# Optimization experiments

Measured on AMD Instinct MI355X. Metric: run time of the kernel, lower is better.

## Reference

```python
import jax, jax.numpy as jnp
import numpy as np

F_DIM = 128
H_DIM = 64
N_NODES = 100000
N_EDGES = 1000000
BN_EPS = 1e-5

def setup_inputs() -> dict:
    key = jax.random.key(0)
    ks = jax.random.split(key, 10)
    x = jax.random.normal(ks[0], (N_NODES, F_DIM), dtype=jnp.float32)
    edges = jax.random.randint(ks[1], (2, N_EDGES), 0, N_NODES, dtype=jnp.int64)
    s_in = 1.0 / np.sqrt(2 * F_DIM)
    s_h = 1.0 / np.sqrt(H_DIM)
    W_in = jax.random.uniform(ks[2], (H_DIM, 2 * F_DIM), jnp.float32, -s_in, s_in)
    b_in = jax.random.uniform(ks[3], (H_DIM,), jnp.float32, -s_in, s_in)
    W_h = jax.random.uniform(ks[4], (H_DIM, H_DIM), jnp.float32, -s_h, s_h)
    b_h = jax.random.uniform(ks[5], (H_DIM,), jnp.float32, -s_h, s_h)
    gamma = jnp.ones((H_DIM,), jnp.float32)
    beta = jnp.zeros((H_DIM,), jnp.float32)
    W_out = jax.random.uniform(ks[6], (1, H_DIM), jnp.float32, -s_h, s_h)
    b_out = jax.random.uniform(ks[7], (1,), jnp.float32, -s_h, s_h)
    return {"x": x, "edges": edges, "W_in": W_in, "b_in": b_in,
            "W_h": W_h, "b_h": b_h, "gamma": gamma, "beta": beta,
            "W_out": W_out, "b_out": b_out}

def reference(x, edges, W_in, b_in, W_h, b_h, gamma, beta, W_out, b_out):
    # gather node pair features and concat -> [E, 2F]
    ef = jnp.concatenate((x[edges[0]], x[edges[1]]), axis=1)
    h = jax.nn.relu(ef @ W_in.T + b_in)          # [E, H]
    h = h @ W_h.T + b_h                           # hidden linear
    # BatchNorm1d in training mode: batch stats over edge dim (biased var)
    mean = jnp.mean(h, axis=0)
    var = jnp.mean((h - mean) ** 2, axis=0)
    h = (h - mean) * jax.lax.rsqrt(var + BN_EPS) * gamma + beta
    h = jax.nn.relu(h)
    edge_scores = (h @ W_out.T + b_out).squeeze(-1)  # [E]
    return edge_scores
```

## Files before the change

### kernel.cpp

```cpp
#include <hip/hip_runtime.h>
#include <hip/hip_bf16.h>
#include <hip/hip_fp16.h>

#define N_NODES 100000
#define N_EDGES 1000000
#define BN_EPS 1e-5f
#define N_CHUNKS (N_EDGES / 64)

typedef __attribute__((ext_vector_type(8))) short bf16x8;
typedef __attribute__((ext_vector_type(4))) float f32x4;


__device__ __forceinline__ unsigned pk2(float a, float b) {
  unsigned ua = __builtin_bit_cast(unsigned, a);
  unsigned ub = __builtin_bit_cast(unsigned, b);
  ua += 0x7fffu + ((ua >> 16) & 1u);
  ub += 0x7fffu + ((ub >> 16) & 1u);
  return (ua >> 16) | (ub & 0xffff0000u);
}

__device__ __forceinline__ bf16x8 pack8(float4 v0, float4 v1) {
  uint4 u = make_uint4(pk2(v0.x, v0.y), pk2(v0.z, v0.w), pk2(v1.x, v1.y), pk2(v1.z, v1.w));
  return __builtin_bit_cast(bf16x8, u);
}

__device__ __forceinline__ bf16x8 frag_relu_add(uint4 a, uint4 d) {
  uint4 r;
  const unsigned* aw = (const unsigned*)&a;
  const unsigned* dw = (const unsigned*)&d;
  unsigned* rw = (unsigned*)&r;
#pragma unroll
  for (int q = 0; q < 4; ++q) {
    const float alo = __builtin_bit_cast(float, aw[q] << 16);
    const float ahi = __builtin_bit_cast(float, aw[q] & 0xffff0000u);
    const float dlo = __builtin_bit_cast(float, dw[q] << 16);
    const float dhi = __builtin_bit_cast(float, dw[q] & 0xffff0000u);
    rw[q] = pk2(fmaxf(alo + dlo, 0.f), fmaxf(ahi + dhi, 0.f));
  }
  return __builtin_bit_cast(bf16x8, r);
}

__device__ __forceinline__ void load_bfr(const float* __restrict__ W_h, int l15, int l4,
                                         bf16x8 bfr[4][2]) {
#pragma unroll
  for (int nt = 0; nt < 4; ++nt)
#pragma unroll
    for (int kk = 0; kk < 2; ++kk) {
      const float* wp = W_h + (16 * nt + l15) * 64 + (kk * 4 + l4) * 8;
      bfr[nt][kk] = pack8(*(const float4*)wp, *(const float4*)(wp + 4));
    }
}

__global__ __launch_bounds__(64) void k_probe(const unsigned* __restrict__ eu,
                                              int* __restrict__ flag) {
  if (threadIdx.x == 0) {
    unsigned acc = 0;
#pragma unroll
    for (int i = 1; i < 64; i += 2) acc |= eu[i];
    *flag = (acc == 0) ? 1 : 0;
  }
}

__global__ __launch_bounds__(256) void k1_mfma(
    const float* __restrict__ x, const float* __restrict__ W_in,
    const float* __restrict__ b_in, __hip_bfloat16* __restrict__ A,
    float* __restrict__ stats) {
  const int t = threadIdx.x;
  if (blockIdx.x == 0 && t < 128) stats[t] = 0.f;
  const int lane = t & 63;
  const int w = t >> 6;
  const int l15 = lane & 15, l4 = lane >> 4;
  const int nb = blockIdx.x * 128 + (w >> 1) * 64;
  const int cb = (w & 1) * 64;

  bf16x8 wfrag[4][4];
#pragma unroll
  for (int ct = 0; ct < 4; ++ct) {
#pragma unroll
    for (int kk = 0; kk < 4; ++kk) {
      const float* wp = W_in + (16 * ct + l15) * 256 + (cb ? 128 : 0) + 32 * kk + 8 * l4;
      wfrag[ct][kk] = pack8(*(const float4*)wp, *(const float4*)(wp + 4));
    }
  }
  f32x4 acc[4][4];
#pragma unroll
  for (int nt = 0; nt < 4; ++nt)
#pragma unroll
    for (int ct = 0; ct < 4; ++ct)
      acc[nt][ct] = (f32x4){0.f, 0.f, 0.f, 0.f};

#pragma unroll
  for (int nt = 0; nt < 4; ++nt) {
    int node = nb + 16 * nt + l15;
    node = node < N_NODES ? node : N_NODES - 1;
    const float* xr = x + (size_t)node * 128 + 8 * l4;
#pragma unroll
    for (int kk = 0; kk < 4; ++kk) {
      const bf16x8 xf = pack8(*(const float4*)(xr + 32 * kk), *(const float4*)(xr + 32 * kk + 4));
#pragma unroll
      for (int ct = 0; ct < 4; ++ct)
        acc[nt][ct] = __builtin_amdgcn_mfma_f32_16x16x32_bf16(wfrag[ct][kk], xf, acc[nt][ct], 0, 0, 0);
    }
  }

  float4 bv[4];
#pragma unroll
  for (int ct = 0; ct < 4; ++ct)
    bv[ct] = cb ? make_float4(0.f, 0.f, 0.f, 0.f) : *(const float4*)(b_in + 16 * ct + 4 * l4);
#pragma unroll
  for (int nt = 0; nt < 4; ++nt) {
    const int node = nb + 16 * nt + l15;
    if (node < N_NODES) {
      __hip_bfloat16* ap = A + (size_t)node * 128 + cb + 4 * l4;
#pragma unroll
      for (int ct = 0; ct < 4; ++ct) {
        uint2 u;
        u.x = pk2(acc[nt][ct][0] + bv[ct].x, acc[nt][ct][1] + bv[ct].y);
        u.y = pk2(acc[nt][ct][2] + bv[ct].z, acc[nt][ct][3] + bv[ct].w);
        *(uint2*)(ap + 16 * ct) = u;
      }
    }
  }
}

template<bool STORE_G>
__global__ __launch_bounds__(256, 2) void k2_stats(
    const __hip_bfloat16* __restrict__ A, const void* __restrict__ edges,
    const int* __restrict__ flag, const float* __restrict__ W_h,
    float* __restrict__ stats, __half* __restrict__ g) {
  const int lane = threadIdx.x & 63;
  const int l15 = lane & 15, l4 = lane >> 4;
  bf16x8 bfr[4][2];
  load_bfr(W_h, l15, l4, bfr);

  const int is64 = *flag;
  const long long* e64 = (const long long*)edges;
  const int* e32 = (const int*)edges;
  float vs[4] = {0.f, 0.f, 0.f, 0.f};
  float vq[4] = {0.f, 0.f, 0.f, 0.f};
  const int gwave = blockIdx.x * 4 + (threadIdx.x >> 6);
  const int nwaves = gridDim.x * 4;

  for (int c = gwave; c < N_CHUNKS; c += 2 * nwaves) {
    const int cy = c + nwaves;
    const bool has2 = cy < N_CHUNKS;
    int sX[4], dX[4], sY[4], dY[4];
#pragma unroll
    for (int mt = 0; mt < 4; ++mt) {
      const int ex = c * 64 + mt * 16 + l15;
      if (is64) { sX[mt] = (int)e64[ex]; dX[mt] = (int)e64[N_EDGES + ex]; }
      else      { sX[mt] = e32[ex];      dX[mt] = e32[N_EDGES + ex]; }
    }
    const int cyc = has2 ? cy : c;
#pragma unroll
    for (int mt = 0; mt < 4; ++mt) {
      const int ey = cyc * 64 + mt * 16 + l15;
      if (is64) { sY[mt] = (int)e64[ey]; dY[mt] = (int)e64[N_EDGES + ey]; }
      else      { sY[mt] = e32[ey];      dY[mt] = e32[N_EDGES + ey]; }
    }
    uint4 xs0[4], xs1[4], xd0[4], xd1[4];
    uint4 ys0[4], ys1[4], yd0[4], yd1[4];
#pragma unroll
    for (int mt = 0; mt < 4; ++mt) {
      const uint4* As = (const uint4*)(A + (size_t)sX[mt] * 128);
      const uint4* Ad = (const uint4*)(A + (size_t)dX[mt] * 128 + 64);
      xs0[mt] = As[l4]; xs1[mt] = As[4 + l4];
      xd0[mt] = Ad[l4]; xd1[mt] = Ad[4 + l4];
    }
#pragma unroll
    for (int mt = 0; mt < 4; ++mt) {
      const uint4* As = (const uint4*)(A + (size_t)sY[mt] * 128);
      const uint4* Ad = (const uint4*)(A + (size_t)dY[mt] * 128 + 64);
      ys0[mt] = As[l4]; ys1[mt] = As[4 + l4];
      yd0[mt] = Ad[l4]; yd1[mt] = Ad[4 + l4];
    }
#pragma unroll
    for (int mt = 0; mt < 4; ++mt) {
      const bf16x8 a0 = frag_relu_add(xs0[mt], xd0[mt]);
      const bf16x8 a1 = frag_relu_add(xs1[mt], xd1[mt]);
#pragma unroll
      for (int nt = 0; nt < 4; ++nt) {
        f32x4 cc = {0.f, 0.f, 0.f, 0.f};
        cc = __builtin_amdgcn_mfma_f32_16x16x32_bf16(a0, bfr[nt][0], cc, 0, 0, 0);
        cc = __builtin_amdgcn_mfma_f32_16x16x32_bf16(a1, bfr[nt][1], cc, 0, 0, 0);
        if (STORE_G) {
          uint2 u;
          u.x = __builtin_bit_cast(unsigned, __floats2half2_rn(cc[0], cc[1]));
          u.y = __builtin_bit_cast(unsigned, __floats2half2_rn(cc[2], cc[3]));
          *(uint2*)(g + ((((size_t)c * 4 + mt) * 4 + nt) * 64 + lane) * 4) = u;
        }
#pragma unroll
        for (int j = 0; j < 4; ++j) { vs[nt] += cc[j]; vq[nt] += cc[j] * cc[j]; }
      }
    }
    if (has2) {
#pragma unroll
      for (int mt = 0; mt < 4; ++mt) {
        const bf16x8 a0 = frag_relu_add(ys0[mt], yd0[mt]);
        const bf16x8 a1 = frag_relu_add(ys1[mt], yd1[mt]);
#pragma unroll
        for (int nt = 0; nt < 4; ++nt) {
          f32x4 cc = {0.f, 0.f, 0.f, 0.f};
          cc = __builtin_amdgcn_mfma_f32_16x16x32_bf16(a0, bfr[nt][0], cc, 0, 0, 0);
          cc = __builtin_amdgcn_mfma_f32_16x16x32_bf16(a1, bfr[nt][1], cc, 0, 0, 0);
          if (STORE_G) {
            uint2 u;
            u.x = __builtin_bit_cast(unsigned, __floats2half2_rn(cc[0], cc[1]));
            u.y = __builtin_bit_cast(unsigned, __floats2half2_rn(cc[2], cc[3]));
            *(uint2*)(g + ((((size_t)cy * 4 + mt) * 4 + nt) * 64 + lane) * 4) = u;
          }
#pragma unroll
          for (int j = 0; j < 4; ++j) { vs[nt] += cc[j]; vq[nt] += cc[j] * cc[j]; }
        }
      }
    }
  }
#pragma unroll
  for (int nt = 0; nt < 4; ++nt) {
    float s1 = vs[nt], s2 = vq[nt];
    s1 += __shfl_xor(s1, 16, 64); s1 += __shfl_xor(s1, 32, 64);
    s2 += __shfl_xor(s2, 16, 64); s2 += __shfl_xor(s2, 32, 64);
    if (lane < 16) {
      atomicAdd(&stats[lane + 16 * nt], s1);
      atomicAdd(&stats[64 + lane + 16 * nt], s2);
    }
  }
}

__global__ __launch_bounds__(64) void k3_finalize(
    const float* __restrict__ stats, const float* __restrict__ gamma,
    const float* __restrict__ beta, float* __restrict__ ss) {
  const int c = threadIdx.x;
  if (c < 64) {
    const float inv_e = 1.f / (float)N_EDGES;
    const float mg = stats[c] * inv_e;
    const float var = stats[64 + c] * inv_e - mg * mg;
    const float scale = gamma[c] * rsqrtf(var + BN_EPS);
    ss[c] = scale;
    ss[64 + c] = beta[c] - scale * mg;
  }
}

__global__ __launch_bounds__(256) void k4_stream(
    const __half* __restrict__ g, const float* __restrict__ ss,
    const float* __restrict__ W_out, const float* __restrict__ b_out,
    float* __restrict__ out) {
  const int lane = threadIdx.x & 63;
  const int l15 = lane & 15, l4 = lane >> 4;
  float scl[4], shf[4], wo[4];
#pragma unroll
  for (int nt = 0; nt < 4; ++nt) {
    scl[nt] = ss[l15 + 16 * nt];
    shf[nt] = ss[64 + l15 + 16 * nt];
    wo[nt] = W_out[l15 + 16 * nt];
  }
  const float bo = b_out[0];
  const int gwave = blockIdx.x * 4 + (threadIdx.x >> 6);
  const int nwaves = gridDim.x * 4;
  for (int chunk = gwave; chunk < N_CHUNKS; chunk += nwaves) {
#pragma unroll
    for (int mt = 0; mt < 4; ++mt) {
      float t0 = 0.f, t1 = 0.f, t2 = 0.f, t3 = 0.f;
#pragma unroll
      for (int nt = 0; nt < 4; ++nt) {
        const uint2 u = *(const uint2*)(g + ((((size_t)chunk * 4 + mt) * 4 + nt) * 64 + lane) * 4);
        const __half2 h0 = __builtin_bit_cast(__half2, u.x);
        const __half2 h1 = __builtin_bit_cast(__half2, u.y);
        t0 += fmaxf(fmaf(__low2float(h0),  scl[nt], shf[nt]), 0.f) * wo[nt];
        t1 += fmaxf(fmaf(__high2float(h0), scl[nt], shf[nt]), 0.f) * wo[nt];
        t2 += fmaxf(fmaf(__low2float(h1),  scl[nt], shf[nt]), 0.f) * wo[nt];
        t3 += fmaxf(fmaf(__high2float(h1), scl[nt], shf[nt]), 0.f) * wo[nt];
      }
      const int ebase = chunk * 64 + mt * 16 + 4 * l4;
#pragma unroll
      for (int j = 0; j < 4; ++j) {
        float r = (j == 0) ? t0 : (j == 1) ? t1 : (j == 2) ? t2 : t3;
        r += __shfl_xor(r, 1, 64);
        r += __shfl_xor(r, 2, 64);
        r += __shfl_xor(r, 4, 64);
        r += __shfl_xor(r, 8, 64);
        if (l15 == 0) out[ebase + j] = r + bo;
      }
    }
  }
}

__global__ __launch_bounds__(256) void k4_gather(
    const __hip_bfloat16* __restrict__ A, const void* __restrict__ edges,
    const int* __restrict__ flag, const float* __restrict__ W_h,
    const float* __restrict__ ss, const float* __restrict__ W_out,
    const float* __restrict__ b_out, float* __restrict__ out) {
  const int lane = threadIdx.x & 63;
  const int l15 = lane & 15, l4 = lane >> 4;
  bf16x8 bfr[4][2];
  load_bfr(W_h, l15, l4, bfr);
  float scl[4], shf[4], wo[4];
#pragma unroll
  for (int nt = 0; nt < 4; ++nt) {
    scl[nt] = ss[l15 + 16 * nt];
    shf[nt] = ss[64 + l15 + 16 * nt];
    wo[nt] = W_out[l15 + 16 * nt];
  }
  const float bo = b_out[0];
  const int is64 = *flag;
  const long long* e64 = (const long long*)edges;
  const int* e32 = (const int*)edges;
  const int gwave = blockIdx.x * 4 + (threadIdx.x >> 6);
  const int nwaves = gridDim.x * 4;
  for (int chunk = gwave; chunk < N_CHUNKS; chunk += nwaves) {
    const int base = chunk * 64;
#pragma unroll
    for (int mt = 0; mt < 4; ++mt) {
      const int eidx = base + mt * 16 + l15;
      int s, d;
      if (is64) { s = (int)e64[eidx]; d = (int)e64[N_EDGES + eidx]; }
      else      { s = e32[eidx];      d = e32[N_EDGES + eidx]; }
      const uint4* As = (const uint4*)(A + (size_t)s * 128);
      const uint4* Ad = (const uint4*)(A + (size_t)d * 128 + 64);
      const bf16x8 a0 = frag_relu_add(As[l4], Ad[l4]);
      const bf16x8 a1 = frag_relu_add(As[4 + l4], Ad[4 + l4]);
      float t0 = 0.f, t1 = 0.f, t2 = 0.f, t3 = 0.f;
#pragma unroll
      for (int nt = 0; nt < 4; ++nt) {
        f32x4 cc = {0.f, 0.f, 0.f, 0.f};
        cc = __builtin_amdgcn_mfma_f32_16x16x32_bf16(a0, bfr[nt][0], cc, 0, 0, 0);
        cc = __builtin_amdgcn_mfma_f32_16x16x32_bf16(a1, bfr[nt][1], cc, 0, 0, 0);
        t0 += fmaxf(fmaf(cc[0], scl[nt], shf[nt]), 0.f) * wo[nt];
        t1 += fmaxf(fmaf(cc[1], scl[nt], shf[nt]), 0.f) * wo[nt];
        t2 += fmaxf(fmaf(cc[2], scl[nt], shf[nt]), 0.f) * wo[nt];
        t3 += fmaxf(fmaf(cc[3], scl[nt], shf[nt]), 0.f) * wo[nt];
      }
      const int ebase = base + mt * 16 + 4 * l4;
#pragma unroll
      for (int j = 0; j < 4; ++j) {
        float r = (j == 0) ? t0 : (j == 1) ? t1 : (j == 2) ? t2 : t3;
        r += __shfl_xor(r, 1, 64);
        r += __shfl_xor(r, 2, 64);
        r += __shfl_xor(r, 4, 64);
        r += __shfl_xor(r, 8, 64);
        if (l15 == 0) out[ebase + j] = r + bo;
      }
    }
  }
}

extern "C" void kernel_launch(void* const* d_in, const int* in_sizes, int n_in,
                              void* d_out, int out_size, void* d_ws, size_t ws_size,
                              hipStream_t stream) {
  const float* x     = (const float*)d_in[0];
  const void*  edges = d_in[1];
  const float* W_in  = (const float*)d_in[2];
  const float* b_in  = (const float*)d_in[3];
  const float* W_h   = (const float*)d_in[4];
  const float* gamma = (const float*)d_in[6];
  const float* beta  = (const float*)d_in[7];
  const float* W_out = (const float*)d_in[8];
  const float* b_out = (const float*)d_in[9];
  float* out = (float*)d_out;

  char* base = (char*)d_ws;
  __hip_bfloat16* A = (__hip_bfloat16*)base;
  const size_t offMeta = (size_t)N_NODES * 128 * sizeof(__hip_bfloat16);
  float* stats = (float*)(base + offMeta);
  float* ss    = stats + 128;
  int*   flag  = (int*)(base + offMeta + 1024);
  __half* g = (__half*)(base + offMeta + 4096);
  const bool use_g = ws_size >= offMeta + 4096 + (size_t)N_EDGES * 64 * sizeof(__half);

  k_probe<<<1, 64, 0, stream>>>((const unsigned*)edges, flag);
  k1_mfma<<<782, 256, 0, stream>>>(x, W_in, b_in, A, stats);
  if (use_g) {
    k2_stats<true><<<976, 256, 0, stream>>>(A, edges, flag, W_h, stats, g);
    k3_finalize<<<1, 64, 0, stream>>>(stats, gamma, beta, ss);
    k4_stream<<<1024, 256, 0, stream>>>(g, ss, W_out, b_out, out);
  } else {
    k2_stats<false><<<976, 256, 0, stream>>>(A, edges, flag, W_h, stats, g);
    k3_finalize<<<1, 64, 0, stream>>>(stats, gamma, beta, ss);
    k4_gather<<<1024, 256, 0, stream>>>(A, edges, flag, W_h, ss, W_out, b_out, out);
  }
}
```

Baseline: 201.6 us.

## Sort edges by source node to localize gathers, scatter outputs back

Adds a counting sort of edges by source node (histogram, scan, scatter) that writes packed src/dst/edge-id pairs. The stats kernel walks the sorted list, split into eight XCD-aligned ranges, so that source-row gathers of A hit cache. The output kernel scatters scores back to their original edge positions, and g stores and loads become nontemporal. This costs several extra kernel launches, a serial single-block scan and atomic-heavy passes over the edge list, all to improve gather locality.

```diff
diff --git a/kernel.cpp b/kernel.cpp
--- a/kernel.cpp
+++ b/kernel.cpp
@@ -51,6 +51,13 @@
     }
 }
 
+__device__ __forceinline__ bool probe_is64(const void* edges) {
+  const unsigned* eu = (const unsigned*)edges;
+  const int lane = threadIdx.x & 63;
+  unsigned pw = (lane < 32) ? eu[2 * lane + 1] : 0u;
+  return __ballot(pw != 0) == 0;
+}
+
 __global__ __launch_bounds__(64) void k_probe(const unsigned* __restrict__ eu,
                                               int* __restrict__ flag) {
   if (threadIdx.x == 0) {
@@ -58,6 +65,65 @@
 #pragma unroll
     for (int i = 1; i < 64; i += 2) acc |= eu[i];
     *flag = (acc == 0) ? 1 : 0;
+  }
+}
+
+__global__ __launch_bounds__(256) void k_zero(unsigned* __restrict__ cnt,
+                                              float* __restrict__ stats) {
+  for (int i = blockIdx.x * 256 + threadIdx.x; i < N_NODES; i += gridDim.x * 256) cnt[i] = 0u;
+  if (blockIdx.x == 0 && threadIdx.x < 128) stats[threadIdx.x] = 0.f;
+}
+
+__global__ __launch_bounds__(256) void k_hist(const void* __restrict__ edges,
+                                              unsigned* __restrict__ cnt) {
+  const bool is64 = probe_is64(edges);
+  const long long* e64 = (const long long*)edges;
+  const int* e32 = (const int*)edges;
+  for (int e = blockIdx.x * 256 + threadIdx.x; e < N_EDGES; e += gridDim.x * 256) {
+    const int s = is64 ? (int)e64[e] : e32[e];
+    atomicAdd(&cnt[s], 1u);
+  }
+}
+
+__global__ __launch_bounds__(1024) void k_scan(const unsigned* __restrict__ cnt,
+                                               unsigned* __restrict__ basev,
+                                               int* __restrict__ cb8) {
+  __shared__ unsigned part[1024];
+  const int t = threadIdx.x;
+  const int s0 = t * 98;
+  const int s1 = (s0 + 98 < N_NODES) ? s0 + 98 : N_NODES;
+  unsigned sum = 0;
+  for (int i = s0; i < s1; ++i) sum += cnt[i];
+  part[t] = sum;
+  __syncthreads();
+  for (int off = 1; off < 1024; off <<= 1) {
+    unsigned v = (t >= off) ? part[t - off] : 0u;
+    __syncthreads();
+    part[t] += v;
+    __syncthreads();
+  }
+  unsigned run = part[t] - sum;
+  for (int i = s0; i < s1; ++i) { const unsigned c = cnt[i]; basev[i] = run; run += c; }
+  __syncthreads();
+  if (t < 8) cb8[t] = (int)(basev[t * 12500] >> 6);
+  if (t == 8) cb8[8] = N_CHUNKS;
+}
+
+__global__ __launch_bounds__(256) void k_scatter(const void* __restrict__ edges,
+                                                 unsigned* __restrict__ basev,
+                                                 int2* __restrict__ sd) {
+  const bool is64 = probe_is64(edges);
+  const long long* e64 = (const long long*)edges;
+  const int* e32 = (const int*)edges;
+  for (int e = blockIdx.x * 256 + threadIdx.x; e < N_EDGES; e += gridDim.x * 256) {
+    int s, d;
+    if (is64) { s = (int)e64[e]; d = (int)e64[N_EDGES + e]; }
+    else      { s = e32[e];      d = e32[N_EDGES + e]; }
+    const unsigned pos = atomicAdd(&basev[s], 1u);
+    int2 p;
+    p.x = s | ((e & 0x7FFF) << 17);
+    p.y = d | ((e >> 15) << 17);
+    sd[pos] = p;
   }
 }
 
@@ -123,40 +189,37 @@
   }
 }
 
-template<bool STORE_G>
-__global__ __launch_bounds__(256, 2) void k2_stats(
-    const __hip_bfloat16* __restrict__ A, const void* __restrict__ edges,
-    const int* __restrict__ flag, const float* __restrict__ W_h,
+__global__ __launch_bounds__(256, 2) void k2s_stats(
+    const __hip_bfloat16* __restrict__ A, const int2* __restrict__ sd,
+    const int* __restrict__ cb8, const float* __restrict__ W_h,
     float* __restrict__ stats, __half* __restrict__ g) {
   const int lane = threadIdx.x & 63;
   const int l15 = lane & 15, l4 = lane >> 4;
   bf16x8 bfr[4][2];
   load_bfr(W_h, l15, l4, bfr);
 
-  const int is64 = *flag;
-  const long long* e64 = (const long long*)edges;
-  const int* e32 = (const int*)edges;
+  const int xb = blockIdx.x & 7;
+  const int start = cb8[xb], end = cb8[xb + 1];
+  const int gw = (blockIdx.x >> 3) * 4 + (threadIdx.x >> 6);
+  const int nw = (gridDim.x >> 3) * 4;
   float vs[4] = {0.f, 0.f, 0.f, 0.f};
   float vq[4] = {0.f, 0.f, 0.f, 0.f};
-  const int gwave = blockIdx.x * 4 + (threadIdx.x >> 6);
-  const int nwaves = gridDim.x * 4;
-
-  for (int c = gwave; c < N_CHUNKS; c += 2 * nwaves) {
-    const int cy = c + nwaves;
-    const bool has2 = cy < N_CHUNKS;
+
+  for (int i = start + gw; i < end; i += 2 * nw) {
+    const int c = i;
+    const int cy = i + nw;
+    const bool has2 = cy < end;
     int sX[4], dX[4], sY[4], dY[4];
 #pragma unroll
     for (int mt = 0; mt < 4; ++mt) {
-      const int ex = c * 64 + mt * 16 + l15;
-      if (is64) { sX[mt] = (int)e64[ex]; dX[mt] = (int)e64[N_EDGES + ex]; }
-      else      { sX[mt] = e32[ex];      dX[mt] = e32[N_EDGES + ex]; }
+      const int2 p = sd[c * 64 + mt * 16 + l15];
+      sX[mt] = p.x & 0x1FFFF; dX[mt] = p.y & 0x1FFFF;
     }
     const int cyc = has2 ? cy : c;
 #pragma unroll
     for (int mt = 0; mt < 4; ++mt) {
-      const int ey = cyc * 64 + mt * 16 + l15;
-      if (is64) { sY[mt] = (int)e64[ey]; dY[mt] = (int)e64[N_EDGES + ey]; }
-      else      { sY[mt] = e32[ey];      dY[mt] = e32[N_EDGES + ey]; }
+      const int2 p = sd[cyc * 64 + mt * 16 + l15];
+      sY[mt] = p.x & 0x1FFFF; dY[mt] = p.y & 0x1FFFF;
     }
     uint4 xs0[4], xs1[4], xd0[4], xd1[4];
     uint4 ys0[4], ys1[4], yd0[4], yd1[4];
@@ -183,12 +246,11 @@
         f32x4 cc = {0.f, 0.f, 0.f, 0.f};
         cc = __builtin_amdgcn_mfma_f32_16x16x32_bf16(a0, bfr[nt][0], cc, 0, 0, 0);
         cc = __builtin_amdgcn_mfma_f32_16x16x32_bf16(a1, bfr[nt][1], cc, 0, 0, 0);
-        if (STORE_G) {
-          uint2 u;
-          u.x = __builtin_bit_cast(unsigned, __floats2half2_rn(cc[0], cc[1]));
-          u.y = __builtin_bit_cast(unsigned, __floats2half2_rn(cc[2], cc[3]));
-          *(uint2*)(g + ((((size_t)c * 4 + mt) * 4 + nt) * 64 + lane) * 4) = u;
-        }
+        uint2 u;
+        u.x = __builtin_bit_cast(unsigned, __floats2half2_rn(cc[0], cc[1]));
+        u.y = __builtin_bit_cast(unsigned, __floats2half2_rn(cc[2], cc[3]));
+        __builtin_nontemporal_store(*(unsigned long long*)&u,
+            (unsigned long long*)(g + ((((size_t)c * 4 + mt) * 4 + nt) * 64 + lane) * 4));
 #pragma unroll
         for (int j = 0; j < 4; ++j) { vs[nt] += cc[j]; vq[nt] += cc[j] * cc[j]; }
       }
@@ -203,12 +265,11 @@
           f32x4 cc = {0.f, 0.f, 0.f, 0.f};
           cc = __builtin_amdgcn_mfma_f32_16x16x32_bf16(a0, bfr[nt][0], cc, 0, 0, 0);
           cc = __builtin_amdgcn_mfma_f32_16x16x32_bf16(a1, bfr[nt][1], cc, 0, 0, 0);
-          if (STORE_G) {
-            uint2 u;
-            u.x = __builtin_bit_cast(unsigned, __floats2half2_rn(cc[0], cc[1]));
-            u.y = __builtin_bit_cast(unsigned, __floats2half2_rn(cc[2], cc[3]));
-            *(uint2*)(g + ((((size_t)cy * 4 + mt) * 4 + nt) * 64 + lane) * 4) = u;
-          }
+          uint2 u;
+          u.x = __builtin_bit_cast(unsigned, __floats2half2_rn(cc[0], cc[1]));
+          u.y = __builtin_bit_cast(unsigned, __floats2half2_rn(cc[2], cc[3]));
+          __builtin_nontemporal_store(*(unsigned long long*)&u,
+              (unsigned long long*)(g + ((((size_t)cy * 4 + mt) * 4 + nt) * 64 + lane) * 4));
 #pragma unroll
           for (int j = 0; j < 4; ++j) { vs[nt] += cc[j]; vq[nt] += cc[j] * cc[j]; }
         }
@@ -238,6 +299,162 @@
     const float scale = gamma[c] * rsqrtf(var + BN_EPS);
     ss[c] = scale;
     ss[64 + c] = beta[c] - scale * mg;
+  }
+}
+
+__global__ __launch_bounds__(256) void k4s_out(
+    const __half* __restrict__ g, const int2* __restrict__ sd,
+    const float* __restrict__ ss, const float* __restrict__ W_out,
+    const float* __restrict__ b_out, float* __restrict__ out) {
+  const int lane = threadIdx.x & 63;
+  const int l15 = lane & 15, l4 = lane >> 4;
+  float scl[4], shf[4], wo[4];
+#pragma unroll
+  for (int nt = 0; nt < 4; ++nt) {
+    scl[nt] = ss[l15 + 16 * nt];
+    shf[nt] = ss[64 + l15 + 16 * nt];
+    wo[nt] = W_out[l15 + 16 * nt];
+  }
+  const float bo = b_out[0];
+  const int gwave = blockIdx.x * 4 + (threadIdx.x >> 6);
+  const int nwaves = gridDim.x * 4;
+  for (int chunk = gwave; chunk < N_CHUNKS; chunk += nwaves) {
+#pragma unroll
+    for (int mt = 0; mt < 4; ++mt) {
+      float t0 = 0.f, t1 = 0.f, t2 = 0.f, t3 = 0.f;
+#pragma unroll
+      for (int nt = 0; nt < 4; ++nt) {
+        const unsigned long long uv = __builtin_nontemporal_load(
+            (const unsigned long long*)(g + ((((size_t)chunk * 4 + mt) * 4 + nt) * 64 + lane) * 4));
+        const __half2 h0 = __builtin_bit_cast(__half2, (unsigned)(uv & 0xffffffffu));
+        const __half2 h1 = __builtin_bit_cast(__half2, (unsigned)(uv >> 32));
+        t0 += fmaxf(fmaf(__low2float(h0),  scl[nt], shf[nt]), 0.f) * wo[nt];
+        t1 += fmaxf(fmaf(__high2float(h0), scl[nt], shf[nt]), 0.f) * wo[nt];
+        t2 += fmaxf(fmaf(__low2float(h1),  scl[nt], shf[nt]), 0.f) * wo[nt];
+        t3 += fmaxf(fmaf(__high2float(h1), scl[nt], shf[nt]), 0.f) * wo[nt];
+      }
+      float rr[4];
+#pragma unroll
+      for (int j = 0; j < 4; ++j) {
+        float r = (j == 0) ? t0 : (j == 1) ? t1 : (j == 2) ? t2 : t3;
+        r += __shfl_xor(r, 1, 64);
+        r += __shfl_xor(r, 2, 64);
+        r += __shfl_xor(r, 4, 64);
+        r += __shfl_xor(r, 8, 64);
+        rr[j] = r + bo;
+      }
+      if (l15 == 0) {
+        const int ebase = chunk * 64 + mt * 16 + 4 * l4;
+#pragma unroll
+        for (int j = 0; j < 4; ++j) {
+          const int2 p = sd[ebase + j];
+          const int e = (int)(((unsigned)p.x >> 17) | (((unsigned)p.y >> 17) << 15));
+          out[e] = rr[j];
+        }
+      }
+    }
+  }
+}
+
+template<bool STORE_G>
+__global__ __launch_bounds__(256, 2) void k2_stats(
+    const __hip_bfloat16* __restrict__ A, const void* __restrict__ edges,
+    const int* __restrict__ flag, const float* __restrict__ W_h,
+    float* __restrict__ stats, __half* __restrict__ g) {
+  const int lane = threadIdx.x & 63;
+  const int l15 = lane & 15, l4 = lane >> 4;
+  bf16x8 bfr[4][2];
+  load_bfr(W_h, l15, l4, bfr);
+  const int is64 = *flag;
+  const long long* e64 = (const long long*)edges;
+  const int* e32 = (const int*)edges;
+  float vs[4] = {0.f, 0.f, 0.f, 0.f};
+  float vq[4] = {0.f, 0.f, 0.f, 0.f};
+  const int gwave = blockIdx.x * 4 + (threadIdx.x >> 6);
+  const int nwaves = gridDim.x * 4;
+  for (int c = gwave; c < N_CHUNKS; c += 2 * nwaves) {
+    const int cy = c + nwaves;
+    const bool has2 = cy < N_CHUNKS;
+    int sX[4], dX[4], sY[4], dY[4];
+#pragma unroll
+    for (int mt = 0; mt < 4; ++mt) {
+      const int ex = c * 64 + mt * 16 + l15;
+      if (is64) { sX[mt] = (int)e64[ex]; dX[mt] = (int)e64[N_EDGES + ex]; }
+      else      { sX[mt] = e32[ex];      dX[mt] = e32[N_EDGES + ex]; }
+    }
+    const int cyc = has2 ? cy : c;
+#pragma unroll
+    for (int mt = 0; mt < 4; ++mt) {
+      const int ey = cyc * 64 + mt * 16 + l15;
+      if (is64) { sY[mt] = (int)e64[ey]; dY[mt] = (int)e64[N_EDGES + ey]; }
+      else      { sY[mt] = e32[ey];      dY[mt] = e32[N_EDGES + ey]; }
+    }
+    uint4 xs0[4], xs1[4], xd0[4], xd1[4];
+    uint4 ys0[4], ys1[4], yd0[4], yd1[4];
+#pragma unroll
+    for (int mt = 0; mt < 4; ++mt) {
+      const uint4* As = (const uint4*)(A + (size_t)sX[mt] * 128);
+      const uint4* Ad = (const uint4*)(A + (size_t)dX[mt] * 128 + 64);
+      xs0[mt] = As[l4]; xs1[mt] = As[4 + l4];
+      xd0[mt] = Ad[l4]; xd1[mt] = Ad[4 + l4];
+    }
+#pragma unroll
+    for (int mt = 0; mt < 4; ++mt) {
+      const uint4* As = (const uint4*)(A + (size_t)sY[mt] * 128);
+      const uint4* Ad = (const uint4*)(A + (size_t)dY[mt] * 128 + 64);
+      ys0[mt] = As[l4]; ys1[mt] = As[4 + l4];
+      yd0[mt] = Ad[l4]; yd1[mt] = Ad[4 + l4];
+    }
+#pragma unroll
+    for (int mt = 0; mt < 4; ++mt) {
+      const bf16x8 a0 = frag_relu_add(xs0[mt], xd0[mt]);
+      const bf16x8 a1 = frag_relu_add(xs1[mt], xd1[mt]);
+#pragma unroll
+      for (int nt = 0; nt < 4; ++nt) {
+        f32x4 cc = {0.f, 0.f, 0.f, 0.f};
+        cc = __builtin_amdgcn_mfma_f32_16x16x32_bf16(a0, bfr[nt][0], cc, 0, 0, 0);
+        cc = __builtin_amdgcn_mfma_f32_16x16x32_bf16(a1, bfr[nt][1], cc, 0, 0, 0);
+        if (STORE_G) {
+          uint2 u;
+          u.x = __builtin_bit_cast(unsigned, __floats2half2_rn(cc[0], cc[1]));
+          u.y = __builtin_bit_cast(unsigned, __floats2half2_rn(cc[2], cc[3]));
+          *(uint2*)(g + ((((size_t)c * 4 + mt) * 4 + nt) * 64 + lane) * 4) = u;
+        }
+#pragma unroll
+        for (int j = 0; j < 4; ++j) { vs[nt] += cc[j]; vq[nt] += cc[j] * cc[j]; }
+      }
+    }
+    if (has2) {
+#pragma unroll
+      for (int mt = 0; mt < 4; ++mt) {
+        const bf16x8 a0 = frag_relu_add(ys0[mt], yd0[mt]);
+        const bf16x8 a1 = frag_relu_add(ys1[mt], yd1[mt]);
+#pragma unroll
+        for (int nt = 0; nt < 4; ++nt) {
+          f32x4 cc = {0.f, 0.f, 0.f, 0.f};
+          cc = __builtin_amdgcn_mfma_f32_16x16x32_bf16(a0, bfr[nt][0], cc, 0, 0, 0);
+          cc = __builtin_amdgcn_mfma_f32_16x16x32_bf16(a1, bfr[nt][1], cc, 0, 0, 0);
+          if (STORE_G) {
+            uint2 u;
+            u.x = __builtin_bit_cast(unsigned, __floats2half2_rn(cc[0], cc[1]));
+            u.y = __builtin_bit_cast(unsigned, __floats2half2_rn(cc[2], cc[3]));
+            *(uint2*)(g + ((((size_t)cy * 4 + mt) * 4 + nt) * 64 + lane) * 4) = u;
+          }
+#pragma unroll
+          for (int j = 0; j < 4; ++j) { vs[nt] += cc[j]; vq[nt] += cc[j] * cc[j]; }
+        }
+      }
+    }
+  }
+#pragma unroll
+  for (int nt = 0; nt < 4; ++nt) {
+    float s1 = vs[nt], s2 = vq[nt];
+    s1 += __shfl_xor(s1, 16, 64); s1 += __shfl_xor(s1, 32, 64);
+    s2 += __shfl_xor(s2, 16, 64); s2 += __shfl_xor(s2, 32, 64);
+    if (lane < 16) {
+      atomicAdd(&stats[lane + 16 * nt], s1);
+      atomicAdd(&stats[64 + lane + 16 * nt], s2);
+    }
   }
 }
 
@@ -364,16 +581,34 @@
   float* stats = (float*)(base + offMeta);
   float* ss    = stats + 128;
   int*   flag  = (int*)(base + offMeta + 1024);
-  __half* g = (__half*)(base + offMeta + 4096);
-  const bool use_g = ws_size >= offMeta + 4096 + (size_t)N_EDGES * 64 * sizeof(__half);
-
-  k_probe<<<1, 64, 0, stream>>>((const unsigned*)edges, flag);
-  k1_mfma<<<782, 256, 0, stream>>>(x, W_in, b_in, A, stats);
-  if (use_g) {
+  int*   cb8   = (int*)(base + offMeta + 1088);
+  const size_t offG = offMeta + 4096;
+  __half* g = (__half*)(base + offG);
+  unsigned* cnt   = (unsigned*)(base + offG);
+  unsigned* basev = cnt + N_NODES;
+  const size_t offSd = offG + (size_t)N_EDGES * 64 * sizeof(__half);
+  int2* sd = (int2*)(base + offSd);
+  const size_t needSorted = offSd + (size_t)N_EDGES * sizeof(int2);
+  const size_t needG = offSd;
+
+  if (ws_size >= needSorted) {
+    k_zero<<<128, 256, 0, stream>>>(cnt, stats);
+    k_hist<<<512, 256, 0, stream>>>(edges, cnt);
+    k_scan<<<1, 1024, 0, stream>>>(cnt, basev, cb8);
+    k_scatter<<<512, 256, 0, stream>>>(edges, basev, sd);
+    k1_mfma<<<782, 256, 0, stream>>>(x, W_in, b_in, A, stats);
+    k2s_stats<<<2048, 256, 0, stream>>>(A, sd, cb8, W_h, stats, g);
+    k3_finalize<<<1, 64, 0, stream>>>(stats, gamma, beta, ss);
+    k4s_out<<<2048, 256, 0, stream>>>(g, sd, ss, W_out, b_out, out);
+  } else if (ws_size >= needG) {
+    k_probe<<<1, 64, 0, stream>>>((const unsigned*)edges, flag);
+    k1_mfma<<<782, 256, 0, stream>>>(x, W_in, b_in, A, stats);
     k2_stats<true><<<976, 256, 0, stream>>>(A, edges, flag, W_h, stats, g);
     k3_finalize<<<1, 64, 0, stream>>>(stats, gamma, beta, ss);
     k4_stream<<<1024, 256, 0, stream>>>(g, ss, W_out, b_out, out);
   } else {
+    k_probe<<<1, 64, 0, stream>>>((const unsigned*)edges, flag);
+    k1_mfma<<<782, 256, 0, stream>>>(x, W_in, b_in, A, stats);
     k2_stats<false><<<976, 256, 0, stream>>>(A, edges, flag, W_h, stats, g);
     k3_finalize<<<1, 64, 0, stream>>>(stats, gamma, beta, ss);
     k4_gather<<<1024, 256, 0, stream>>>(A, edges, flag, W_h, ss, W_out, b_out, out);
```

New measurement: 596.9 us. +196.0%, slower.
